# Optimization experiments

Measured on AMD Instinct MI355X. Metric: run time of the kernel, lower is better.

The kernel has to match this reference:

```python
import jax, jax.numpy as jnp
import numpy as np

B, T, I, H, K, U = 16, 256, 64, 128, 64, 256
NOISE_INIT = 0.1

def lecun_tanh(x):
    return 1.7159 * jnp.tanh(0.666 * x)

def setup_inputs() -> dict:
    key = jax.random.key(0)
    ks = jax.random.split(key, 16)
    s_in = 1.0 / np.sqrt(I + H)
    s_bb = 1.0 / np.sqrt(U)
    inp = {
        "x": jax.random.normal(ks[0], (B, T, I), dtype=jnp.float32),
        "timespans": jax.random.uniform(ks[1], (B, T), dtype=jnp.float32, minval=0.05, maxval=1.0),
        "noise_eps": jax.random.normal(ks[2], (T, B, K, H), dtype=jnp.float32),
        # backbone: Linear(I+H -> U)
        "Wb": jax.random.normal(ks[3], (I + H, U), dtype=jnp.float32) * s_in,
        "bb": jnp.zeros((U,), dtype=jnp.float32),
        # CfC heads: Linear(U -> H) each
        "W_ff1": jax.random.normal(ks[4], (U, H), dtype=jnp.float32) * s_bb,
        "b_ff1": jnp.zeros((H,), dtype=jnp.float32),
        "W_ff2": jax.random.normal(ks[5], (U, H), dtype=jnp.float32) * s_bb,
        "b_ff2": jnp.zeros((H,), dtype=jnp.float32),
        "W_ta": jax.random.normal(ks[6], (U, H), dtype=jnp.float32) * s_bb,
        "b_ta": jnp.zeros((H,), dtype=jnp.float32),
        "W_tb": jax.random.normal(ks[7], (U, H), dtype=jnp.float32) * s_bb,
        "b_tb": jnp.zeros((H,), dtype=jnp.float32),
        # learnable time-scaled noise scale (per hidden unit)
        "noise_scale": jnp.full((H,), NOISE_INIT, dtype=jnp.float32),
    }
    return inp


def reference(x, timespans, noise_eps, Wb, bb, W_ff1, b_ff1, W_ff2, b_ff2,
              W_ta, b_ta, W_tb, b_tb, noise_scale):
    # initial particle state: zeros, uniform log-weights
    particles0 = jnp.zeros((B, K, H), dtype=x.dtype)
    log_w0 = jnp.full((B, K), -jnp.log(jnp.asarray(K, x.dtype)), dtype=x.dtype)

    def step(carry, inputs):
        particles, log_w = carry
        x_t, ts_t, eps_t = inputs  # [B,I], [B], [B,K,H]
        ts = ts_t[:, None, None]                                  # [B,1,1]
        xk = jnp.broadcast_to(x_t[:, None, :], (B, K, I))
        z = jnp.concatenate([xk, particles], axis=-1)             # [B,K,I+H]
        bbk = lecun_tanh(jnp.einsum('bku,uv->bkv', z, Wb) + bb)   # backbone [B,K,U]
        ff1 = jnp.tanh(jnp.einsum('bku,uh->bkh', bbk, W_ff1) + b_ff1)
        ff2 = jnp.tanh(jnp.einsum('bku,uh->bkh', bbk, W_ff2) + b_ff2)
        t_a = jnp.einsum('bku,uh->bkh', bbk, W_ta) + b_ta
        t_b = jnp.einsum('bku,uh->bkh', bbk, W_tb) + b_tb
        t_interp = jax.nn.sigmoid(t_a * ts + t_b)                 # CfC gate
        new_p = ff1 * (1.0 - t_interp) + t_interp * ff2           # [B,K,H]
        # time-scaled state noise injection
        new_p = new_p + noise_scale * jnp.sqrt(ts) * eps_t
        # weights stay uniform (no observations) -> ESS = K, no resampling
        w = jax.nn.softmax(log_w, axis=-1)                        # [B,K]
        out = jnp.einsum('bk,bkh->bh', w, new_p)                  # weighted mean
        return (new_p, log_w), out

    x_t = jnp.transpose(x, (1, 0, 2))        # [T,B,I]
    ts_t = jnp.transpose(timespans, (1, 0))  # [T,B]
    (particles, log_w), outs = jax.lax.scan(step, (particles0, log_w0),
                                            (x_t, ts_t, noise_eps))
    outputs = jnp.transpose(outs, (1, 0, 2))  # [B,T,H]
    return outputs, particles, log_w
```

## Files before the change

kernel.cpp:

```cpp
#include <hip/hip_runtime.h>
#include <math.h>

typedef __attribute__((ext_vector_type(8))) short short8;
typedef __attribute__((ext_vector_type(4))) float f32x4;

#define B_ 16
#define T_ 256
#define I_ 64
#define H_ 128
#define K_ 64
#define U_ 256
#define KC 16
#define NTHR 512

#define OUT_OFF_P (B_*T_*H_)
#define OUT_OFF_LW (OUT_OFF_P + B_*K_*H_)

__device__ __forceinline__ unsigned short f2bf(float x) {
    unsigned int u = __float_as_uint(x);
    u += 0x7fffu + ((u >> 16) & 1u);
    return (unsigned short)(u >> 16);
}
__device__ __forceinline__ float bf2f(unsigned short u) {
    return __uint_as_float(((unsigned int)u) << 16);
}
__device__ __forceinline__ float fast_tanh(float x) {
    float e = __expf(2.0f * x);
    return 1.0f - 2.0f * __builtin_amdgcn_rcpf(e + 1.0f);
}
__device__ __forceinline__ float fast_sigmoid(float x) {
    return __builtin_amdgcn_rcpf(1.0f + __expf(-x));
}
__device__ __forceinline__ unsigned int swzbyte_p(unsigned int row, unsigned int col) {
    return (row * 256u + col * 2u) ^ ((row & 7u) << 4);
}
__device__ __forceinline__ unsigned int swzbyte_b(unsigned int row, unsigned int pos) {
    return (row * 512u + pos * 2u) ^ ((row & 7u) << 4);
}

#define BAR() do { asm volatile("s_waitcnt lgkmcnt(0)" ::: "memory"); \
                   __builtin_amdgcn_s_barrier(); \
                   asm volatile("" ::: "memory"); } while (0)

#define MFMA16(a, bfrag, c) __builtin_amdgcn_mfma_f32_16x16x32_bf16((a), (bfrag), (c), 0, 0, 0)

__global__ __launch_bounds__(256) void xw_kernel(
    const float* __restrict__ x, const float* __restrict__ Wb,
    const float* __restrict__ bb, unsigned short* __restrict__ xw)
{
    const int tid  = threadIdx.x;
    const int lane = tid & 63;
    const int wv   = tid >> 6;
    const int ln15 = lane & 15;
    const int l4   = lane >> 4;
    const int bid  = blockIdx.x;
    const int b    = bid >> 4;
    const int t0   = (bid & 15) * 16;

    short8 Bx[2][4];
    float bbc[4];
    #pragma unroll
    for (int kt = 0; kt < 2; ++kt) {
        #pragma unroll
        for (int ct = 0; ct < 4; ++ct) {
            short8 f;
            const int col = wv * 64 + ct * 16 + ln15;
            #pragma unroll
            for (int j = 0; j < 8; ++j)
                f[j] = (short)f2bf(Wb[(kt * 32 + l4 * 8 + j) * U_ + col]);
            Bx[kt][ct] = f;
        }
    }
    #pragma unroll
    for (int ct = 0; ct < 4; ++ct) bbc[ct] = bb[wv * 64 + ct * 16 + ln15];

    short8 ax[2];
    #pragma unroll
    for (int kt = 0; kt < 2; ++kt) {
        const float* xp = &x[(size_t)(b * T_ + t0 + ln15) * I_ + kt * 32 + l4 * 8];
        short8 f;
        #pragma unroll
        for (int j = 0; j < 8; ++j) f[j] = (short)f2bf(xp[j]);
        ax[kt] = f;
    }
    const f32x4 z4 = {0.f, 0.f, 0.f, 0.f};
    f32x4 acc[4] = {z4, z4, z4, z4};
    #pragma unroll
    for (int kt = 0; kt < 2; ++kt) {
        #pragma unroll
        for (int ct = 0; ct < 4; ++ct) acc[ct] = MFMA16(ax[kt], Bx[kt][ct], acc[ct]);
    }
    #pragma unroll
    for (int ct = 0; ct < 4; ++ct) {
        #pragma unroll
        for (int r = 0; r < 4; ++r) {
            const int trow = t0 + l4 * 4 + r;
            xw[(size_t)(b * T_ + trow) * U_ + wv * 64 + ct * 16 + ln15] = f2bf(acc[ct][r] + bbc[ct]);
        }
    }
}

__global__ __launch_bounds__(NTHR, 2) void pf_kernel(
    const unsigned short* __restrict__ xw, const float* __restrict__ tspan,
    const float* __restrict__ eps, const float* __restrict__ Wb,
    const float* __restrict__ Wf1, const float* __restrict__ bf1,
    const float* __restrict__ Wf2, const float* __restrict__ bf2,
    const float* __restrict__ Wta, const float* __restrict__ bta,
    const float* __restrict__ Wtb, const float* __restrict__ btb,
    const float* __restrict__ nscale, float* __restrict__ out)
{
    const int tid  = threadIdx.x;
    const int lane = tid & 63;
    const int wv   = tid >> 6;
    const int ln15 = lane & 15;
    const int l4   = lane >> 4;
    const int bid  = blockIdx.x;
    const int b    = bid >> 2;
    const int k0   = (bid & 3) * KC;

    __shared__ unsigned short p_bf[KC * H_];
    __shared__ unsigned short bbk_bf[KC * U_];
    __shared__ float ts_lds[T_];

    for (int i = tid; i < KC * H_; i += NTHR) p_bf[i] = 0;
    for (int i = tid; i < T_; i += NTHR) ts_lds[i] = tspan[b * T_ + i];

    short8 B1p[4][2];
    #pragma unroll
    for (int kt = 0; kt < 4; ++kt) {
        #pragma unroll
        for (int ct = 0; ct < 2; ++ct) {
            short8 f;
            const int col = wv * 32 + ct * 16 + ln15;
            #pragma unroll
            for (int j = 0; j < 8; ++j)
                f[j] = (short)f2bf(Wb[(I_ + kt * 32 + l4 * 8 + j) * U_ + col]);
            B1p[kt][ct] = f;
        }
    }
    const float* Whp[4] = {Wf1, Wf2, Wta, Wtb};
    const int hc = wv * 16 + ln15;
    short8 B2[4][8];
    #pragma unroll
    for (int hd = 0; hd < 4; ++hd) {
        #pragma unroll
        for (int kt = 0; kt < 8; ++kt) {
            short8 f;
            #pragma unroll
            for (int j = 0; j < 8; ++j) {
                const int pos = l4 * 8 + j;
                const int kg  = kt * 32 + (pos >> 1) + ((pos & 1) << 4);
                f[j] = (short)f2bf(Whp[hd][kg * H_ + hc]);
            }
            B2[hd][kt] = f;
        }
    }
    const float bf1c = bf1[hc], bf2c = bf2[hc];
    const float btac = bta[hc], btbc = btb[hc];
    const float nscc = nscale[hc];

    if ((bid & 3) == 0 && tid < K_)
        out[OUT_OFF_LW + b * K_ + tid] = -4.1588830833596715f;

    __syncthreads();

    const float* ep0 = eps + ((size_t)(b * K_ + k0 + l4 * 4)) * H_ + hc;
    const unsigned short* xwp = xw + (size_t)b * T_ * U_ + wv * 32 + ln15;
    float ecur[4];
    #pragma unroll
    for (int r = 0; r < 4; ++r) ecur[r] = ep0[r * H_];
    float xw0c = bf2f(xwp[0]), xw1c = bf2f(xwp[16]);
    float tscur = ts_lds[0];

    const f32x4 zero4 = {0.f, 0.f, 0.f, 0.f};

    for (int t = 0; t < T_; ++t) {
        const int tn = (t + 1 < T_) ? t + 1 : t;
        const float* epn = ep0 + (size_t)tn * (B_ * K_ * H_);
        float enext[4];
        #pragma unroll
        for (int r = 0; r < 4; ++r) enext[r] = epn[r * H_];
        const float xw0n = bf2f(xwp[tn * U_]), xw1n = bf2f(xwp[tn * U_ + 16]);
        const float tsn = ts_lds[tn];

        f32x4 acc0 = {xw0c, xw0c, xw0c, xw0c};
        f32x4 acc1 = {xw1c, xw1c, xw1c, xw1c};
        #pragma unroll
        for (int kt = 0; kt < 4; ++kt) {
            const short8 ap = *(const short8*)((const char*)p_bf + swzbyte_p(ln15, kt * 32 + l4 * 8));
            acc0 = MFMA16(ap, B1p[kt][0], acc0);
            acc1 = MFMA16(ap, B1p[kt][1], acc1);
        }
        #pragma unroll
        for (int r = 0; r < 4; ++r) {
            const int row = l4 * 4 + r;
            const unsigned int q0 = f2bf(1.7159f * fast_tanh(0.666f * acc0[r]));
            const unsigned int q1 = f2bf(1.7159f * fast_tanh(0.666f * acc1[r]));
            *(unsigned int*)((char*)bbk_bf + swzbyte_b(row, wv * 32 + 2 * ln15)) = q0 | (q1 << 16);
        }
        BAR();

        f32x4 a_f1 = zero4, a_f2 = zero4, a_ta = zero4, a_tb = zero4;
        #pragma unroll
        for (int kt = 0; kt < 8; ++kt) {
            const short8 a = *(const short8*)((const char*)bbk_bf + swzbyte_b(ln15, kt * 32 + l4 * 8));
            a_f1 = MFMA16(a, B2[0][kt], a_f1);
            a_f2 = MFMA16(a, B2[1][kt], a_f2);
            a_ta = MFMA16(a, B2[2][kt], a_ta);
            a_tb = MFMA16(a, B2[3][kt], a_tb);
        }
        const float sq = sqrtf(tscur);
        float psum = 0.f;
        const bool last = (t == T_ - 1);
        #pragma unroll
        for (int r = 0; r < 4; ++r) {
            const int row = l4 * 4 + r;
            const float f1v = fast_tanh(a_f1[r] + bf1c);
            const float f2v = fast_tanh(a_f2[r] + bf2c);
            const float tiv = fast_sigmoid((a_ta[r] + btac) * tscur + (a_tb[r] + btbc));
            const float np  = f1v + tiv * (f2v - f1v) + nscc * sq * ecur[r];
            *(unsigned short*)((char*)p_bf + swzbyte_p(row, hc)) = f2bf(np);
            psum += np;
            if (last)
                out[OUT_OFF_P + (size_t)(b * K_ + k0 + row) * H_ + hc] = np;
        }
        psum += __shfl_xor(psum, 16);
        psum += __shfl_xor(psum, 32);
        if (lane < 16)
            atomicAdd(&out[(size_t)(b * T_ + t) * H_ + wv * 16 + lane], psum * (1.0f / 64.0f));

        #pragma unroll
        for (int r = 0; r < 4; ++r) ecur[r] = enext[r];
        xw0c = xw0n; xw1c = xw1n;
        tscur = tsn;
        BAR();
    }
}

extern "C" void kernel_launch(void* const* d_in, const int* in_sizes, int n_in,
                              void* d_out, int out_size, void* d_ws, size_t ws_size,
                              hipStream_t stream) {
    const float* x    = (const float*)d_in[0];
    const float* tsp  = (const float*)d_in[1];
    const float* eps  = (const float*)d_in[2];
    const float* Wb   = (const float*)d_in[3];
    const float* bb   = (const float*)d_in[4];
    const float* Wf1  = (const float*)d_in[5];
    const float* bf1  = (const float*)d_in[6];
    const float* Wf2  = (const float*)d_in[7];
    const float* bf2  = (const float*)d_in[8];
    const float* Wta  = (const float*)d_in[9];
    const float* bta  = (const float*)d_in[10];
    const float* Wtb  = (const float*)d_in[11];
    const float* btb  = (const float*)d_in[12];
    const float* nsc  = (const float*)d_in[13];
    float* out = (float*)d_out;
    unsigned short* xw = (unsigned short*)d_ws;

    (void)hipMemsetAsync(d_out, 0, (size_t)OUT_OFF_P * sizeof(float), stream);
    xw_kernel<<<dim3(256), dim3(256), 0, stream>>>(x, Wb, bb, xw);
    pf_kernel<<<dim3(64), dim3(NTHR), 0, stream>>>(
        xw, tsp, eps, Wb, Wf1, bf1, Wf2, bf2, Wta, bta, Wtb, btb, nsc, out);
}
```

Measured before the change: 493.9 us.

## Defer per-step mean reduction, use hardware bf16 pack, widen LDS swizzle

The cross-lane reduction and atomicAdd of each step's particle mean now run at the start of the next iteration, so the shuffles overlap with the following step's work rather than sitting right before the barrier. Backbone activations are packed to bf16 with the v_cvt_pk_bf16_f32 instruction instead of manual integer rounding. The LDS swizzle also XORs bit 3 of the row to cut more bank conflicts on the MFMA fragment reads. The loop is forced not to unroll, and the last step's reduction is handled after the loop.

```diff
diff --git a/kernel.cpp b/kernel.cpp
--- a/kernel.cpp
+++ b/kernel.cpp
@@ -24,6 +24,11 @@
 __device__ __forceinline__ float bf2f(unsigned short u) {
     return __uint_as_float(((unsigned int)u) << 16);
 }
+__device__ __forceinline__ unsigned int cvt_pk_bf16(float lo, float hi) {
+    unsigned int pk;
+    asm("v_cvt_pk_bf16_f32 %0, %1, %2" : "=v"(pk) : "v"(lo), "v"(hi));
+    return pk;
+}
 __device__ __forceinline__ float fast_tanh(float x) {
     float e = __expf(2.0f * x);
     return 1.0f - 2.0f * __builtin_amdgcn_rcpf(e + 1.0f);
@@ -32,10 +37,10 @@
     return __builtin_amdgcn_rcpf(1.0f + __expf(-x));
 }
 __device__ __forceinline__ unsigned int swzbyte_p(unsigned int row, unsigned int col) {
-    return (row * 256u + col * 2u) ^ ((row & 7u) << 4);
+    return (row * 256u + col * 2u) ^ ((row & 7u) << 4) ^ ((row & 8u) << 2);
 }
 __device__ __forceinline__ unsigned int swzbyte_b(unsigned int row, unsigned int pos) {
-    return (row * 512u + pos * 2u) ^ ((row & 7u) << 4);
+    return (row * 512u + pos * 2u) ^ ((row & 7u) << 4) ^ ((row & 8u) << 2);
 }
 
 #define BAR() do { asm volatile("s_waitcnt lgkmcnt(0)" ::: "memory"); \
@@ -173,8 +178,18 @@
     float tscur = ts_lds[0];
 
     const f32x4 zero4 = {0.f, 0.f, 0.f, 0.f};
-
+    float psum_d = 0.f;
+
+    #pragma unroll 1
     for (int t = 0; t < T_; ++t) {
+        if (t) {
+            float ps = psum_d;
+            ps += __shfl_xor(ps, 16);
+            ps += __shfl_xor(ps, 32);
+            if (lane < 16)
+                atomicAdd(&out[(size_t)(b * T_ + (t - 1)) * H_ + wv * 16 + lane], ps * (1.0f / 64.0f));
+        }
+
         const int tn = (t + 1 < T_) ? t + 1 : t;
         const float* epn = ep0 + (size_t)tn * (B_ * K_ * H_);
         float enext[4];
@@ -194,9 +209,9 @@
         #pragma unroll
         for (int r = 0; r < 4; ++r) {
             const int row = l4 * 4 + r;
-            const unsigned int q0 = f2bf(1.7159f * fast_tanh(0.666f * acc0[r]));
-            const unsigned int q1 = f2bf(1.7159f * fast_tanh(0.666f * acc1[r]));
-            *(unsigned int*)((char*)bbk_bf + swzbyte_b(row, wv * 32 + 2 * ln15)) = q0 | (q1 << 16);
+            const float v0 = 1.7159f * fast_tanh(0.666f * acc0[r]);
+            const float v1 = 1.7159f * fast_tanh(0.666f * acc1[r]);
+            *(unsigned int*)((char*)bbk_bf + swzbyte_b(row, wv * 32 + 2 * ln15)) = cvt_pk_bf16(v0, v1);
         }
         BAR();
 
@@ -224,16 +239,21 @@
             if (last)
                 out[OUT_OFF_P + (size_t)(b * K_ + k0 + row) * H_ + hc] = np;
         }
-        psum += __shfl_xor(psum, 16);
-        psum += __shfl_xor(psum, 32);
-        if (lane < 16)
-            atomicAdd(&out[(size_t)(b * T_ + t) * H_ + wv * 16 + lane], psum * (1.0f / 64.0f));
+        psum_d = psum;
 
         #pragma unroll
         for (int r = 0; r < 4; ++r) ecur[r] = enext[r];
         xw0c = xw0n; xw1c = xw1n;
         tscur = tsn;
         BAR();
+    }
+
+    {
+        float ps = psum_d;
+        ps += __shfl_xor(ps, 16);
+        ps += __shfl_xor(ps, 32);
+        if (lane < 16)
+            atomicAdd(&out[(size_t)(b * T_ + (T_ - 1)) * H_ + wv * 16 + lane], ps * (1.0f / 64.0f));
     }
 }
 
```

Result: slower. 549.6 us (+11.3%).
